# Performance work log

Measured on AMD Instinct MI355X. Metric: run time of the kernel, lower is better.

## Reference

```python
import jax, jax.numpy as jnp
import numpy as np

N, E, C, H, L, G, K, NC = 50000, 500000, 256, 128, 4, 64, 8, 2
EPS_MSG = 1e-7  # GENConv message eps
EPS_BN = 1e-5   # BatchNorm eps


def setup_inputs() -> dict:
    key = jax.random.key(0)
    ks = jax.random.split(key, 32)
    def nrm(k, shape, scale):
        return jax.random.normal(k, shape, dtype=jnp.float32) * scale
    sC = 1.0 / np.sqrt(C).astype(np.float32)
    sH = 1.0 / np.sqrt(H).astype(np.float32)
    s2H = 1.0 / np.sqrt(2 * H).astype(np.float32)
    return dict(
        x=nrm(ks[0], (N, C), 1.0),
        edge_index=jax.random.randint(ks[1], (2, E), 0, N, dtype=jnp.int32),
        edge_attr=jax.random.uniform(ks[2], (E, 1), dtype=jnp.float32),
        batch=jnp.sort(jax.random.randint(ks[3], (N,), 0, G, dtype=jnp.int32)),
        clinical=nrm(ks[4], (G, K), 1.0),
        lin_src_w=nrm(ks[5], (C, H), sC), lin_src_b=nrm(ks[6], (H,), 0.01),
        lin_dst_w=nrm(ks[7], (C, H), sC), lin_dst_b=nrm(ks[8], (H,), 0.01),
        edge_w=nrm(ks[9], (L, 1, H), 1.0), edge_b=nrm(ks[10], (L, H), 0.01),
        t=0.1 + 0.01 * jax.random.normal(ks[11], (L,), dtype=jnp.float32),
        mlp_w1=nrm(ks[12], (L, H, 2 * H), sH), mlp_b1=nrm(ks[13], (L, 2 * H), 0.01),
        mlp_bn_g=1.0 + nrm(ks[14], (L, 2 * H), 0.1), mlp_bn_b=nrm(ks[15], (L, 2 * H), 0.1),
        mlp_bn_m=nrm(ks[16], (L, 2 * H), 0.1),
        mlp_bn_v=1.0 + jax.random.uniform(ks[17], (L, 2 * H), dtype=jnp.float32),
        mlp_w2=nrm(ks[18], (L, 2 * H, H), s2H), mlp_b2=nrm(ks[19], (L, H), 0.01),
        norm_g=1.0 + nrm(ks[20], (L, H), 0.1), norm_b=nrm(ks[21], (L, H), 0.1),
        norm_m=nrm(ks[22], (L, H), 0.1),
        norm_v=1.0 + jax.random.uniform(ks[23], (L, H), dtype=jnp.float32),
        cls_w=nrm(ks[24], (H + K, NC), 1.0 / np.sqrt(H + K).astype(np.float32)),
        cls_b=nrm(ks[25], (NC,), 0.01),
    )


def _bn(h, g, b, m, v):
    # eval-mode BatchNorm with running stats
    return g * (h - m) * jax.lax.rsqrt(v + EPS_BN) + b


def reference(x, edge_index, edge_attr, batch, clinical,
              lin_src_w, lin_src_b, lin_dst_w, lin_dst_b,
              edge_w, edge_b, t,
              mlp_w1, mlp_b1, mlp_bn_g, mlp_bn_b, mlp_bn_m, mlp_bn_v,
              mlp_w2, mlp_b2, norm_g, norm_b, norm_m, norm_v,
              cls_w, cls_b):
    n = x.shape[0]
    g_count = clinical.shape[0]
    src, dst = edge_index[0], edge_index[1]
    n_layers = t.shape[0]

    def genconv(xs, xd, l):
        # xs: source features feeding messages [N,H]; xd: dst skip features [N,H]
        e = edge_attr @ edge_w[l] + edge_b[l]               # [E,H]
        msg = jax.nn.relu(xs[src] + e) + EPS_MSG            # [E,H]
        z = msg * t[l]
        zmax = jax.ops.segment_max(z, dst, num_segments=n)  # [N,H]
        zmax = jnp.where(jnp.isfinite(zmax), zmax, 0.0)
        ez = jnp.exp(z - zmax[dst])
        denom = jax.ops.segment_sum(ez, dst, num_segments=n)
        agg = jax.ops.segment_sum(msg * ez, dst, num_segments=n) / jnp.maximum(denom, 1e-16)
        out = agg + xd
        # internal MLP [H, 2H, H]: Linear -> BN -> ReLU -> Linear
        hmid = jax.nn.relu(_bn(out @ mlp_w1[l] + mlp_b1[l],
                               mlp_bn_g[l], mlp_bn_b[l], mlp_bn_m[l], mlp_bn_v[l]))
        return hmid @ mlp_w2[l] + mlp_b2[l]

    # layer 0: conv only (per DeepGCN.forward); lin_src / lin_dst project C -> H
    xs0 = x @ lin_src_w + lin_src_b
    xd0 = x @ lin_dst_w + lin_dst_b
    h = genconv(xs0, xd0, 0)

    # layers 1..L-1: res+ block (norm -> act -> conv, residual add); dropout = identity (eval)
    for l in range(1, n_layers):
        r = jax.nn.relu(_bn(h, norm_g[l], norm_b[l], norm_m[l], norm_v[l]))
        h = h + genconv(r, r, l)

    # final norm/act from layer 0
    h = jax.nn.relu(_bn(h, norm_g[0], norm_b[0], norm_m[0], norm_v[0]))

    # global mean pool over graphs
    cnt = jax.ops.segment_sum(jnp.ones((n,), h.dtype), batch, num_segments=g_count)
    pooled = jax.ops.segment_sum(h, batch, num_segments=g_count) / jnp.maximum(cnt, 1.0)[:, None]

    z = jnp.concatenate([pooled, clinical], axis=1)
    return z @ cls_w + cls_b  # [G, num_classes]; squeeze is a no-op for G>1, NC=2
```

## Files before the change

kernel.cpp:

```cpp
#include <hip/hip_runtime.h>
#include <math.h>

#define Nn 50000
#define MPAD 50048
#define Ee 500000
#define Cc 256
#define Hh 128
#define Ll 4
#define Gg 64
#define Kk 8
#define NCc 2

#define NB 196

typedef __attribute__((ext_vector_type(8))) short short8;
typedef __attribute__((ext_vector_type(4))) float f32x4;
typedef __attribute__((ext_vector_type(2))) float f32x2;

#define RFL __builtin_amdgcn_readfirstlane

__device__ __forceinline__ unsigned short f2bf(float f) {
    union { float f; unsigned int u; } v;
    v.f = f;
    unsigned int u = v.u;
    return (unsigned short)((u + 0x7FFFu + ((u >> 16) & 1u)) >> 16);
}
__device__ __forceinline__ float bf2f(unsigned short s) {
    union { float f; unsigned int u; } v;
    v.u = ((unsigned int)s) << 16;
    return v.f;
}
__device__ __forceinline__ float bf2f_lo(unsigned int u) {
    union { float f; unsigned int u; } v;
    v.u = u << 16;
    return v.f;
}
__device__ __forceinline__ float bf2f_hi(unsigned int u) {
    union { float f; unsigned int u; } v;
    v.u = u & 0xffff0000u;
    return v.f;
}


__global__ void hist_kernel(const int* __restrict__ dst, int* __restrict__ deg) {
    int e = blockIdx.x * 256 + threadIdx.x;
    if (e < Ee) atomicAdd(&deg[dst[e]], 1);
}

__global__ __launch_bounds__(256) void bsum_kernel(const int* __restrict__ deg,
                                                   int* __restrict__ bsum) {
    __shared__ int ws[4];
    int t = threadIdx.x;
    int i = blockIdx.x * 256 + t;
    int v = (i < Nn) ? deg[i] : 0;
#pragma unroll
    for (int o = 32; o; o >>= 1) v += __shfl_down(v, o, 64);
    if ((t & 63) == 0) ws[t >> 6] = v;
    __syncthreads();
    if (t == 0) bsum[blockIdx.x] = ws[0] + ws[1] + ws[2] + ws[3];
}

__global__ __launch_bounds__(256) void bscan_kernel(const int* __restrict__ bsum,
                                                    int* __restrict__ boff,
                                                    int* __restrict__ off) {
    __shared__ int sc[256];
    int t = threadIdx.x;
    int v = (t < NB) ? bsum[t] : 0;
    sc[t] = v;
    __syncthreads();
    for (int o = 1; o < 256; o <<= 1) {
        int u = (t >= o) ? sc[t - o] : 0;
        __syncthreads();
        sc[t] += u;
        __syncthreads();
    }
    if (t < NB) boff[t] = sc[t] - v;
    if (t == NB - 1) off[Nn] = sc[t];
}

__global__ __launch_bounds__(256) void offsets_kernel(const int* __restrict__ deg,
                                                      const int* __restrict__ boff,
                                                      int* __restrict__ off,
                                                      int* __restrict__ pos) {
    __shared__ int sc[256];
    int t = threadIdx.x;
    int i = blockIdx.x * 256 + t;
    int v = (i < Nn) ? deg[i] : 0;
    sc[t] = v;
    __syncthreads();
    for (int o = 1; o < 256; o <<= 1) {
        int u = (t >= o) ? sc[t - o] : 0;
        __syncthreads();
        sc[t] += u;
        __syncthreads();
    }
    int excl = sc[t] - v + boff[blockIdx.x];
    if (i < Nn) {
        off[i] = excl;
        pos[i] = excl;
    }
}

__global__ void scatter_kernel(const int* __restrict__ src, const int* __restrict__ dst,
                               const float* __restrict__ attr, int* __restrict__ pos,
                               int2* __restrict__ sedge) {
    int e = blockIdx.x * 256 + threadIdx.x;
    if (e < Ee) {
        int d = dst[e];
        int p = atomicAdd(&pos[d], 1);
        sedge[p] = make_int2(src[e], __float_as_int(attr[e]));
    }
}


__global__ void wconv_kernel(const float* __restrict__ lin_src_w,
                             const float* __restrict__ lin_dst_w,
                             const float* __restrict__ mlp_w1,
                             const float* __restrict__ mlp_w2,
                             unsigned short* __restrict__ wt) {
    int idx = blockIdx.x * 256 + threadIdx.x;
    if (idx >= 327680) return;
    float val;
    if (idx < 65536) {
        int n = idx >> 8, k = idx & 255;
        val = (n < 128) ? lin_src_w[k * 128 + n] : lin_dst_w[k * 128 + (n - 128)];
    } else if (idx < 196608) {
        int r = idx - 65536;
        int l = r >> 15, e = r & 32767;
        int n = e >> 7, k = e & 127;
        val = mlp_w1[(size_t)l * 32768 + k * 256 + n];
    } else {
        int r = idx - 196608;
        int l = r >> 15, e = r & 32767;
        int n = e >> 8, k = e & 255;
        val = mlp_w2[(size_t)l * 32768 + k * 128 + n];
    }
    wt[idx] = f2bf(val);
}


__global__ __launch_bounds__(256) void xconv_kernel(const float* __restrict__ x,
                                                    unsigned short* __restrict__ xbf) {
    int idx = blockIdx.x * 256 + threadIdx.x;
    if (idx >= (Nn * Cc) / 8) return;
    const float4* p = (const float4*)(x) + (size_t)idx * 2;
    float4 v0 = p[0], v1 = p[1];
    unsigned short t[8];
    t[0] = f2bf(v0.x); t[1] = f2bf(v0.y); t[2] = f2bf(v0.z); t[3] = f2bf(v0.w);
    t[4] = f2bf(v1.x); t[5] = f2bf(v1.y); t[6] = f2bf(v1.z); t[7] = f2bf(v1.w);
    *(short8*)(xbf + (size_t)idx * 8) = *(short8*)t;
}

#define GLOAD16(gp, lp)                                                                       \
    __builtin_amdgcn_global_load_lds(                                                         \
        (const __attribute__((address_space(1))) unsigned int*)(gp),                          \
        (__attribute__((address_space(3))) unsigned int*)(lp), 16, 0, 0)


__global__ __launch_bounds__(256) void proj_kernel(
    const unsigned short* __restrict__ A, const unsigned short* __restrict__ Bt,
    const float* __restrict__ bias, const float* __restrict__ bias2,
    unsigned short* __restrict__ Cout) {
    __shared__ __align__(16) unsigned short SH[24576];
    int tid = threadIdx.x;
    int wave = tid >> 6, lane = tid & 63;
    int wr = wave >> 1, wc = wave & 1;
    int lrow = lane & 15, quad = lane >> 4;
    int m0 = blockIdx.y * 128, n0 = blockIdx.x * 128;
    const int K = 256;

    const unsigned short* ag0 = A + (size_t)(m0 + (tid >> 2)) * K + (tid & 3) * 8;
    const unsigned short* ag1 = A + (size_t)(m0 + 64 + (tid >> 2)) * K + (tid & 3) * 8;
    const unsigned short* bg0 = Bt + (size_t)(n0 + (tid >> 2)) * K + (tid & 3) * 8;
    const unsigned short* bg1 = Bt + (size_t)(n0 + 64 + (tid >> 2)) * K + (tid & 3) * 8;

    f32x4 acc[4][4];
#pragma unroll
    for (int i = 0; i < 4; i++)
#pragma unroll
        for (int j = 0; j < 4; j++) acc[i][j] = (f32x4){0.f, 0.f, 0.f, 0.f};

    auto stage = [&](int buf, int koff) {
        GLOAD16(ag0 + koff, SH + buf * 4096 + wave * 512);
        GLOAD16(ag1 + koff, SH + buf * 4096 + 2048 + wave * 512);
        GLOAD16(bg0 + koff, SH + 12288 + buf * 4096 + wave * 512);
        GLOAD16(bg1 + koff, SH + 12288 + buf * 4096 + 2048 + wave * 512);
    };

    const int ntiles = 8;
    stage(0, 0);
    stage(1, 32);
    for (int t = 0; t < ntiles; ++t) {
        if (t + 1 < ntiles) {
            asm volatile("s_waitcnt vmcnt(4)\n\ts_barrier" ::: "memory");
        } else {
            asm volatile("s_waitcnt vmcnt(0)\n\ts_barrier" ::: "memory");
        }
        if (t + 2 < ntiles) stage((t + 2) % 3, (t + 2) * 32);
        int cur = t % 3;
        const unsigned short* As = SH + cur * 4096;
        const unsigned short* Bs = SH + 12288 + cur * 4096;
        short8 af[4], bfr[4];
#pragma unroll
        for (int mt = 0; mt < 4; mt++)
            af[mt] = *(const short8*)&As[(wr * 64 + mt * 16 + lrow) * 32 + quad * 8];
#pragma unroll
        for (int nf = 0; nf < 4; nf++)
            bfr[nf] = *(const short8*)&Bs[(wc * 64 + nf * 16 + lrow) * 32 + quad * 8];
#pragma unroll
        for (int mt = 0; mt < 4; mt++)
#pragma unroll
            for (int nf = 0; nf < 4; nf++)
                acc[mt][nf] = __builtin_amdgcn_mfma_f32_16x16x32_bf16(af[mt], bfr[nf],
                                                                     acc[mt][nf], 0, 0, 0);
    }

    __syncthreads();
    unsigned short* Cl = SH;
#pragma unroll
    for (int nf = 0; nf < 4; nf++) {
        int gc = n0 + wc * 64 + nf * 16 + lrow;
        float bs = (gc >= 128) ? bias2[gc - 128] : bias[gc];
        int col = wc * 64 + nf * 16 + lrow;
#pragma unroll
        for (int mt = 0; mt < 4; mt++)
#pragma unroll
            for (int r = 0; r < 4; r++)
                Cl[(wr * 64 + mt * 16 + quad * 4 + r) * 128 + col] = f2bf(acc[mt][nf][r] + bs);
    }
    __syncthreads();
#pragma unroll
    for (int p = 0; p < 8; p++) {
        int vid = p * 256 + tid;
        int row = vid >> 4, cg = (vid & 15) * 8;
        short8 v = *(const short8*)&Cl[row * 128 + cg];
        *(short8*)(Cout + (size_t)(m0 + row) * 256 + n0 + cg) = v;
    }
}


__global__ __launch_bounds__(256) void mlp_kernel(
    const unsigned short* __restrict__ A,
    const unsigned short* __restrict__ W1,
    const unsigned short* __restrict__ W2,
    const float* __restrict__ b1, const float* __restrict__ bn_g,
    const float* __restrict__ bn_b, const float* __restrict__ bn_m,
    const float* __restrict__ bn_v, const float* __restrict__ b2,
    const float* __restrict__ pn_g, const float* __restrict__ pn_b,
    const float* __restrict__ pn_m, const float* __restrict__ pn_v,
    float* __restrict__ hbuf, unsigned short* __restrict__ rbuf, int rmw) {
    __shared__ __align__(16) unsigned short Hm[64 * 264];

    int tid = threadIdx.x;
    int wave = tid >> 6, lane = tid & 63;
    int lrow = lane & 15, quad = lane >> 4;
    int m0 = blockIdx.x * 64;

    f32x4 acc1[4][4];
#pragma unroll
    for (int i = 0; i < 4; i++)
#pragma unroll
        for (int j = 0; j < 4; j++) acc1[i][j] = (f32x4){0.f, 0.f, 0.f, 0.f};
#pragma unroll
    for (int t = 0; t < 4; t++) {
        short8 af[4], bfr[4];
#pragma unroll
        for (int mt = 0; mt < 4; mt++)
            af[mt] = *(const short8*)(A + (size_t)(m0 + mt * 16 + lrow) * 128 +
                                      t * 32 + quad * 8);
#pragma unroll
        for (int nf = 0; nf < 4; nf++)
            bfr[nf] = *(const short8*)(W1 + (size_t)(wave * 64 + nf * 16 + lrow) * 128 +
                                       t * 32 + quad * 8);
#pragma unroll
        for (int mt = 0; mt < 4; mt++)
#pragma unroll
            for (int nf = 0; nf < 4; nf++)
                acc1[mt][nf] = __builtin_amdgcn_mfma_f32_16x16x32_bf16(af[mt], bfr[nf],
                                                                      acc1[mt][nf], 0, 0, 0);
    }
#pragma unroll
    for (int nf = 0; nf < 4; nf++) {
        int gc = wave * 64 + nf * 16 + lrow;
        float bs = b1[gc];
        float g = bn_g[gc], bb = bn_b[gc], mm = bn_m[gc];
        float inv = rsqrtf(bn_v[gc] + 1e-5f);
#pragma unroll
        for (int mt = 0; mt < 4; mt++)
#pragma unroll
            for (int r = 0; r < 4; r++) {
                float v = acc1[mt][nf][r] + bs;
                v = fmaxf(g * (v - mm) * inv + bb, 0.f);
                Hm[(mt * 16 + quad * 4 + r) * 264 + gc] = f2bf(v);
            }
    }
    __syncthreads();

    f32x4 acc2[4][2];
#pragma unroll
    for (int i = 0; i < 4; i++)
#pragma unroll
        for (int j = 0; j < 2; j++) acc2[i][j] = (f32x4){0.f, 0.f, 0.f, 0.f};
#pragma unroll
    for (int t = 0; t < 8; t++) {
        short8 af[4], bfr[2];
#pragma unroll
        for (int mt = 0; mt < 4; mt++)
            af[mt] = *(const short8*)&Hm[(mt * 16 + lrow) * 264 + t * 32 + quad * 8];
#pragma unroll
        for (int nf = 0; nf < 2; nf++)
            bfr[nf] = *(const short8*)(W2 + (size_t)(wave * 32 + nf * 16 + lrow) * 256 +
                                       t * 32 + quad * 8);
#pragma unroll
        for (int mt = 0; mt < 4; mt++)
#pragma unroll
            for (int nf = 0; nf < 2; nf++)
                acc2[mt][nf] = __builtin_amdgcn_mfma_f32_16x16x32_bf16(af[mt], bfr[nf],
                                                                      acc2[mt][nf], 0, 0, 0);
    }
    __syncthreads();

    float* C2 = (float*)Hm;
#pragma unroll
    for (int nf = 0; nf < 2; nf++) {
        int gc = wave * 32 + nf * 16 + lrow;
        float bs = b2[gc];
#pragma unroll
        for (int mt = 0; mt < 4; mt++)
#pragma unroll
            for (int r = 0; r < 4; r++)
                C2[(mt * 16 + quad * 4 + r) * 132 + gc] = acc2[mt][nf][r] + bs;
    }
    __syncthreads();
#pragma unroll
    for (int p = 0; p < 8; p++) {
        int vid = p * 256 + tid;
        int row = vid >> 5, c4 = (vid & 31) * 4;
        f32x4 v = *(const f32x4*)&C2[row * 132 + c4];
        float* hp = hbuf + (size_t)(m0 + row) * 128 + c4;
        if (rmw) v += *(const f32x4*)hp;
        *(f32x4*)hp = v;
        if (pn_g) {
            f32x4 pg = *(const f32x4*)&pn_g[c4];
            f32x4 pb = *(const f32x4*)&pn_b[c4];
            f32x4 pm = *(const f32x4*)&pn_m[c4];
            f32x4 pv = *(const f32x4*)&pn_v[c4];
            float r0 = fmaxf(pg[0] * (v[0] - pm[0]) * rsqrtf(pv[0] + 1e-5f) + pb[0], 0.f);
            float r1 = fmaxf(pg[1] * (v[1] - pm[1]) * rsqrtf(pv[1] + 1e-5f) + pb[1], 0.f);
            float r2 = fmaxf(pg[2] * (v[2] - pm[2]) * rsqrtf(pv[2] + 1e-5f) + pb[2], 0.f);
            float r3 = fmaxf(pg[3] * (v[3] - pm[3]) * rsqrtf(pv[3] + 1e-5f) + pb[3], 0.f);
            unsigned int w0 = (unsigned int)f2bf(r0) | ((unsigned int)f2bf(r1) << 16);
            unsigned int w1 = (unsigned int)f2bf(r2) | ((unsigned int)f2bf(r3) << 16);
            uint2 pk = make_uint2(w0, w1);
            *(uint2*)(rbuf + (size_t)(m0 + row) * 128 + c4) = pk;
        }
    }
}


template <int XSS>
__global__ __launch_bounds__(256) void agg_kernel(
    const unsigned short* __restrict__ xs,
    const unsigned short* __restrict__ xd, int xds,
    const int2* __restrict__ sedge, const int* __restrict__ off,
    const float* __restrict__ ew, const float* __restrict__ eb,
    const float* __restrict__ tptr, unsigned short* __restrict__ outb) {
    int wave = threadIdx.x >> 6;
    int lane = threadIdx.x & 63;
    int d0 = blockIdx.x * 8 + wave * 2;
    int d1 = d0 + 1;
    int f0 = lane * 2;
    unsigned int uda = *(const unsigned int*)(xd + (size_t)d0 * xds + f0);
    unsigned int udb = *(const unsigned int*)(xd + (size_t)d1 * xds + f0);
    f32x2 wv = *(const f32x2*)(ew + f0);
    f32x2 bv = *(const f32x2*)(eb + f0);
    float c = tptr[0] * 1.44269504088896f;
    const f32x2 zz = {0.f, 0.f};
    int s0a = RFL(off[d0]), s1a = RFL(off[d0 + 1]);
    int s0b = RFL(off[d1]), s1b = RFL(off[d1 + 1]);
    f32x2 dena = {0.f, 0.f}, numa = {0.f, 0.f};
    f32x2 denb = {0.f, 0.f}, numb = {0.f, 0.f};

#define EDGE2(u, av, den, num)                                      \
    {                                                               \
        f32x2 xv = {bf2f_lo(u), bf2f_hi(u)};                        \
        f32x2 m = __builtin_elementwise_max(xv + bv + (av)*wv, zz); \
        f32x2 e;                                                    \
        e.x = __builtin_amdgcn_exp2f(m.x * c);                      \
        e.y = __builtin_amdgcn_exp2f(m.y * c);                      \
        den += e;                                                   \
        num += m * e;                                               \
    }
#define EDGE2M(u, av, mk, den, num)                                 \
    {                                                               \
        f32x2 xv = {bf2f_lo(u), bf2f_hi(u)};                        \
        f32x2 m = __builtin_elementwise_max(xv + bv + (av)*wv, zz); \
        f32x2 e;                                                    \
        e.x = __builtin_amdgcn_exp2f(m.x * c) * (mk);               \
        e.y = __builtin_amdgcn_exp2f(m.y * c) * (mk);               \
        den += e;                                                   \
        num += m * e;                                               \
    }
#define LOADMETA(jv, ii, aa)                                   \
    {                                                          \
        int4 q0 = *(const int4*)(sedge + (jv));                \
        int4 q1 = *(const int4*)(sedge + (jv) + 2);            \
        int4 q2 = *(const int4*)(sedge + (jv) + 4);            \
        int4 q3 = *(const int4*)(sedge + (jv) + 6);            \
        ii[0] = RFL(q0.x); aa[0] = __int_as_float(RFL(q0.y));  \
        ii[1] = RFL(q0.z); aa[1] = __int_as_float(RFL(q0.w));  \
        ii[2] = RFL(q1.x); aa[2] = __int_as_float(RFL(q1.y));  \
        ii[3] = RFL(q1.z); aa[3] = __int_as_float(RFL(q1.w));  \
        ii[4] = RFL(q2.x); aa[4] = __int_as_float(RFL(q2.y));  \
        ii[5] = RFL(q2.z); aa[5] = __int_as_float(RFL(q2.w));  \
        ii[6] = RFL(q3.x); aa[6] = __int_as_float(RFL(q3.y));  \
        ii[7] = RFL(q3.z); aa[7] = __int_as_float(RFL(q3.w));  \
    }
#define GATHER8(ii, uu)                                                          \
    _Pragma("unroll") for (int k = 0; k < 8; k++) uu[k] =                        \
        *(const unsigned int*)(xs + (size_t)ii[k] * XSS + f0);

    int ja = s0a, jb = s0b;
    while (ja + 8 <= s1a && jb + 8 <= s1b) {
        int ia[8], ib[8];
        float aa[8], ab[8];
        LOADMETA(ja, ia, aa)
        LOADMETA(jb, ib, ab)
        unsigned int ua[8], ub[8];
        GATHER8(ia, ua)
        GATHER8(ib, ub)
#pragma unroll
        for (int k = 0; k < 8; k++) EDGE2(ua[k], aa[k], dena, numa)
#pragma unroll
        for (int k = 0; k < 8; k++) EDGE2(ub[k], ab[k], denb, numb)
        ja += 8;
        jb += 8;
    }
    while (ja + 8 <= s1a) {
        int ia[8];
        float aa[8];
        LOADMETA(ja, ia, aa)
        unsigned int ua[8];
        GATHER8(ia, ua)
#pragma unroll
        for (int k = 0; k < 8; k++) EDGE2(ua[k], aa[k], dena, numa)
        ja += 8;
    }
    while (jb + 8 <= s1b) {
        int ib[8];
        float ab[8];
        LOADMETA(jb, ib, ab)
        unsigned int ub[8];
        GATHER8(ib, ub)
#pragma unroll
        for (int k = 0; k < 8; k++) EDGE2(ub[k], ab[k], denb, numb)
        jb += 8;
    }
    if (ja < s1a || jb < s1b) {
        int lasta = (s1a > s0a) ? s1a - 1 : 0;
        int lastb = (s1b > s0b) ? s1b - 1 : 0;
        int ia[8], ib[8];
        float aa[8], ab[8], ma[8], mb[8];
#pragma unroll
        for (int k = 0; k < 8; k++) {
            int jj = ja + k;
            int cl = (jj < s1a) ? jj : lasta;
            int2 p = sedge[cl];
            ia[k] = RFL(p.x);
            aa[k] = __int_as_float(RFL(p.y));
            ma[k] = (jj < s1a) ? 1.f : 0.f;
            jj = jb + k;
            cl = (jj < s1b) ? jj : lastb;
            int2 q = sedge[cl];
            ib[k] = RFL(q.x);
            ab[k] = __int_as_float(RFL(q.y));
            mb[k] = (jj < s1b) ? 1.f : 0.f;
        }
        unsigned int ua[8], ub[8];
        GATHER8(ia, ua)
        GATHER8(ib, ub)
#pragma unroll
        for (int k = 0; k < 8; k++) EDGE2M(ua[k], aa[k], ma[k], dena, numa)
#pragma unroll
        for (int k = 0; k < 8; k++) EDGE2M(ub[k], ab[k], mb[k], denb, numb)
    }
#undef EDGE2
#undef EDGE2M
#undef LOADMETA
#undef GATHER8
    float a0 = (s1a > s0a) ? (numa.x / dena.x + 1e-7f) : 0.f;
    float a1 = (s1a > s0a) ? (numa.y / dena.y + 1e-7f) : 0.f;
    float b0 = (s1b > s0b) ? (numb.x / denb.x + 1e-7f) : 0.f;
    float b1 = (s1b > s0b) ? (numb.y / denb.y + 1e-7f) : 0.f;
    unsigned int lo = f2bf(a0 + bf2f_lo(uda));
    unsigned int hi = f2bf(a1 + bf2f_hi(uda));
    *(unsigned int*)(outb + (size_t)d0 * Hh + f0) = lo | (hi << 16);
    lo = f2bf(b0 + bf2f_lo(udb));
    hi = f2bf(b1 + bf2f_hi(udb));
    *(unsigned int*)(outb + (size_t)d1 * Hh + f0) = lo | (hi << 16);
}


#define PCHUNK 100

__global__ __launch_bounds__(128) void pool_kernel(
    const float* __restrict__ h, const int* __restrict__ batch,
    const float* __restrict__ g, const float* __restrict__ b,
    const float* __restrict__ m, const float* __restrict__ v,
    float* __restrict__ pooled, float* __restrict__ cnt) {
    int hh = threadIdx.x;
    int i0 = blockIdx.x * PCHUNK;
    int i1 = min(i0 + PCHUNK, Nn);
    if (i0 >= Nn) return;
    float gg = g[hh], bb = b[hh], mm = m[hh], inv = rsqrtf(v[hh] + 1e-5f);
    int cur = batch[i0];
    float sum = 0.f, c = 0.f;
    for (int i = i0; i < i1; i++) {
        int gid = batch[i];
        float val = fmaxf(gg * (h[(size_t)i * Hh + hh] - mm) * inv + bb, 0.f);
        if (gid != cur) {
            atomicAdd(&pooled[(size_t)cur * Hh + hh], sum);
            if (hh == 0) atomicAdd(&cnt[cur], c);
            cur = gid;
            sum = 0.f;
            c = 0.f;
        }
        sum += val;
        c += 1.f;
    }
    atomicAdd(&pooled[(size_t)cur * Hh + hh], sum);
    if (hh == 0) atomicAdd(&cnt[cur], c);
}


__global__ __launch_bounds__(128) void cls_kernel(const float* __restrict__ pooled,
                                                  const float* __restrict__ cnt,
                                                  const float* __restrict__ clinical,
                                                  const float* __restrict__ w,
                                                  const float* __restrict__ bias,
                                                  float* __restrict__ out) {
    int t = threadIdx.x;
    int g = t >> 1, c = t & 1;
    float inv = 1.f / fmaxf(cnt[g], 1.f);
    float s = bias[c];
    for (int j = 0; j < Hh; j++) s += pooled[g * Hh + j] * inv * w[j * NCc + c];
    for (int k = 0; k < Kk; k++) s += clinical[g * Kk + k] * w[(Hh + k) * NCc + c];
    out[g * NCc + c] = s;
}


extern "C" void kernel_launch(void* const* d_in, const int* in_sizes, int n_in,
                              void* d_out, int out_size, void* d_ws, size_t ws_size,
                              hipStream_t stream) {
    const float* x = (const float*)d_in[0];
    const int* eidx = (const int*)d_in[1];
    const float* eattr = (const float*)d_in[2];
    const int* batch = (const int*)d_in[3];
    const float* clinical = (const float*)d_in[4];
    const float* lin_src_w = (const float*)d_in[5];
    const float* lin_src_b = (const float*)d_in[6];
    const float* lin_dst_w = (const float*)d_in[7];
    const float* lin_dst_b = (const float*)d_in[8];
    const float* edge_w = (const float*)d_in[9];
    const float* edge_b = (const float*)d_in[10];
    const float* tt = (const float*)d_in[11];
    const float* mlp_w1 = (const float*)d_in[12];
    const float* mlp_b1 = (const float*)d_in[13];
    const float* bn_g = (const float*)d_in[14];
    const float* bn_b = (const float*)d_in[15];
    const float* bn_m = (const float*)d_in[16];
    const float* bn_v = (const float*)d_in[17];
    const float* mlp_w2 = (const float*)d_in[18];
    const float* mlp_b2 = (const float*)d_in[19];
    const float* norm_g = (const float*)d_in[20];
    const float* norm_b = (const float*)d_in[21];
    const float* norm_m = (const float*)d_in[22];
    const float* norm_v = (const float*)d_in[23];
    const float* cls_w = (const float*)d_in[24];
    const float* cls_b = (const float*)d_in[25];
    float* out = (float*)d_out;

    const int* src = eidx;
    const int* dst = eidx + Ee;

    char* ws = (char*)d_ws;
    size_t off_b = 0;
    auto alloc = [&](size_t bytes) -> void* {
        void* p = ws + off_b;
        off_b += (bytes + 255) & ~(size_t)255;
        return p;
    };
    unsigned short* xsd = (unsigned short*)alloc((size_t)MPAD * 256 * 2);
    unsigned short* rbuf = (unsigned short*)alloc((size_t)MPAD * Hh * 2);
    unsigned short* aggout = (unsigned short*)alloc((size_t)MPAD * Hh * 2);
    unsigned short* xbf = (unsigned short*)alloc((size_t)MPAD * 256 * 2);
    float* hbuf = (float*)alloc((size_t)MPAD * Hh * 4);
    int* deg = (int*)alloc((Nn + 1) * 4);
    int* offp = (int*)alloc((Nn + 1) * 4);
    int* pos = (int*)alloc((size_t)Nn * 4);
    int* bsum = (int*)alloc(NB * 4);
    int* boff = (int*)alloc(NB * 4);
    int2* sedge = (int2*)alloc((size_t)Ee * 8);
    float* pooled = (float*)alloc((size_t)Gg * Hh * 4);
    float* cntb = (float*)alloc(Gg * 4);
    unsigned short* wt = (unsigned short*)alloc((size_t)327680 * 2);

    hipMemsetAsync(deg, 0, (Nn + 1) * 4, stream);
    hipMemsetAsync(pooled, 0, (size_t)Gg * Hh * 4, stream);
    hipMemsetAsync(cntb, 0, Gg * 4, stream);

    hist_kernel<<<(Ee + 255) / 256, 256, 0, stream>>>(dst, deg);
    bsum_kernel<<<NB, 256, 0, stream>>>(deg, bsum);
    bscan_kernel<<<1, 256, 0, stream>>>(bsum, boff, offp);
    offsets_kernel<<<NB, 256, 0, stream>>>(deg, boff, offp, pos);
    scatter_kernel<<<(Ee + 255) / 256, 256, 0, stream>>>(src, dst, eattr, pos, sedge);
    wconv_kernel<<<1280, 256, 0, stream>>>(lin_src_w, lin_dst_w, mlp_w1, mlp_w2, wt);
    xconv_kernel<<<(Nn * Cc / 8 + 255) / 256, 256, 0, stream>>>(x, xbf);

    const unsigned short* wt_proj = wt;
    const unsigned short* wt_w1 = wt + 65536;
    const unsigned short* wt_w2 = wt + 196608;

    dim3 gproj(2, MPAD / 128);
    proj_kernel<<<gproj, 256, 0, stream>>>(xbf, wt_proj, lin_src_b, lin_dst_b, xsd);

    for (int l = 0; l < Ll; l++) {
        if (l == 0) {
            agg_kernel<256><<<Nn / 8, 256, 0, stream>>>(xsd, xsd + 128, 256, sedge, offp,
                                                        edge_w + l * Hh, edge_b + l * Hh,
                                                        tt + l, aggout);
        } else {
            agg_kernel<128><<<Nn / 8, 256, 0, stream>>>(rbuf, rbuf, Hh, sedge, offp,
                                                        edge_w + l * Hh, edge_b + l * Hh,
                                                        tt + l, aggout);
        }
        const float* png = (l < Ll - 1) ? (norm_g + (l + 1) * Hh) : nullptr;
        const float* pnb = (l < Ll - 1) ? (norm_b + (l + 1) * Hh) : nullptr;
        const float* pnm = (l < Ll - 1) ? (norm_m + (l + 1) * Hh) : nullptr;
        const float* pnv = (l < Ll - 1) ? (norm_v + (l + 1) * Hh) : nullptr;
        mlp_kernel<<<MPAD / 64, 256, 0, stream>>>(
            aggout, wt_w1 + (size_t)l * 32768, wt_w2 + (size_t)l * 32768,
            mlp_b1 + l * 2 * Hh, bn_g + l * 2 * Hh, bn_b + l * 2 * Hh,
            bn_m + l * 2 * Hh, bn_v + l * 2 * Hh, mlp_b2 + l * Hh,
            png, pnb, pnm, pnv, hbuf, rbuf, (l == 0) ? 0 : 1);
    }

    pool_kernel<<<(Nn + PCHUNK - 1) / PCHUNK, 128, 0, stream>>>(hbuf, batch, norm_g, norm_b,
                                                                norm_m, norm_v, pooled, cntb);
    cls_kernel<<<1, 128, 0, stream>>>(pooled, cntb, clinical, cls_w, cls_b, out);
}
```

Measured before the change: 528.1 us.

## Stage MLP GEMM operands through double-buffered LDS with async global loads

The fused MLP kernel no longer loads A, W1 and W2 fragments straight from global memory into registers. It copies each 32-wide K slice into a double-buffered shared-memory area with GLOAD16 and prefetches the next slice while MFMAs run on the current one. This is meant to hide global load latency and read uncoalesced fragments from LDS instead of global memory. The cost is an extra 40 KB of LDS, which may lower occupancy, plus a __syncthreads per K step. The output staging also moves to the new buffer with an unpadded stride of 128, which may add bank conflicts.

```diff
diff --git a/kernel.cpp b/kernel.cpp
--- a/kernel.cpp
+++ b/kernel.cpp
@@ -249,6 +249,7 @@
     const float* __restrict__ pn_g, const float* __restrict__ pn_b,
     const float* __restrict__ pn_m, const float* __restrict__ pn_v,
     float* __restrict__ hbuf, unsigned short* __restrict__ rbuf, int rmw) {
+    __shared__ __align__(16) unsigned short S[20480];
     __shared__ __align__(16) unsigned short Hm[64 * 264];
 
     int tid = threadIdx.x;
@@ -256,29 +257,46 @@
     int lrow = lane & 15, quad = lane >> 4;
     int m0 = blockIdx.x * 64;
 
+    const unsigned short* ag = A + (size_t)(m0 + (tid >> 2)) * 128 + (tid & 3) * 8;
+    const unsigned short* bg = W1 + (size_t)(tid >> 2) * 128 + (tid & 3) * 8;
+
     f32x4 acc1[4][4];
 #pragma unroll
     for (int i = 0; i < 4; i++)
 #pragma unroll
         for (int j = 0; j < 4; j++) acc1[i][j] = (f32x4){0.f, 0.f, 0.f, 0.f};
-#pragma unroll
-    for (int t = 0; t < 4; t++) {
+
+    auto stage1 = [&](int buf, int k0) {
+        GLOAD16(ag + k0, S + buf * 2048 + wave * 512);
+#pragma unroll
+        for (int c = 0; c < 4; c++)
+            GLOAD16(bg + (size_t)c * 64 * 128 + k0,
+                    S + 4096 + buf * 8192 + c * 2048 + wave * 512);
+    };
+
+    stage1(0, 0);
+    __syncthreads();
+    for (int t = 0; t < 4; ++t) {
+        if (t + 1 < 4) stage1((t + 1) & 1, (t + 1) * 32);
+        int cur = t & 1;
+        const unsigned short* A1s = S + cur * 2048;
+        const unsigned short* B1s = S + 4096 + cur * 8192;
         short8 af[4], bfr[4];
 #pragma unroll
         for (int mt = 0; mt < 4; mt++)
-            af[mt] = *(const short8*)(A + (size_t)(m0 + mt * 16 + lrow) * 128 +
-                                      t * 32 + quad * 8);
+            af[mt] = *(const short8*)&A1s[(mt * 16 + lrow) * 32 + quad * 8];
 #pragma unroll
         for (int nf = 0; nf < 4; nf++)
-            bfr[nf] = *(const short8*)(W1 + (size_t)(wave * 64 + nf * 16 + lrow) * 128 +
-                                       t * 32 + quad * 8);
+            bfr[nf] = *(const short8*)&B1s[(wave * 64 + nf * 16 + lrow) * 32 + quad * 8];
 #pragma unroll
         for (int mt = 0; mt < 4; mt++)
 #pragma unroll
             for (int nf = 0; nf < 4; nf++)
                 acc1[mt][nf] = __builtin_amdgcn_mfma_f32_16x16x32_bf16(af[mt], bfr[nf],
                                                                       acc1[mt][nf], 0, 0, 0);
-    }
+        __syncthreads();
+    }
+
 #pragma unroll
     for (int nf = 0; nf < 4; nf++) {
         int gc = wave * 64 + nf * 16 + lrow;
@@ -296,31 +314,43 @@
     }
     __syncthreads();
 
+    const unsigned short* b2g0 = W2 + (size_t)(tid >> 2) * 256 + (tid & 3) * 8;
+    const unsigned short* b2g1 = W2 + (size_t)(64 + (tid >> 2)) * 256 + (tid & 3) * 8;
+
     f32x4 acc2[4][2];
 #pragma unroll
     for (int i = 0; i < 4; i++)
 #pragma unroll
         for (int j = 0; j < 2; j++) acc2[i][j] = (f32x4){0.f, 0.f, 0.f, 0.f};
-#pragma unroll
-    for (int t = 0; t < 8; t++) {
+
+    auto stage2 = [&](int buf, int k0) {
+        GLOAD16(b2g0 + k0, S + buf * 4096 + wave * 512);
+        GLOAD16(b2g1 + k0, S + buf * 4096 + 2048 + wave * 512);
+    };
+
+    stage2(0, 0);
+    __syncthreads();
+    for (int t = 0; t < 8; ++t) {
+        if (t + 1 < 8) stage2((t + 1) & 1, (t + 1) * 32);
+        int cur = t & 1;
+        const unsigned short* B2s = S + cur * 4096;
         short8 af[4], bfr[2];
 #pragma unroll
         for (int mt = 0; mt < 4; mt++)
             af[mt] = *(const short8*)&Hm[(mt * 16 + lrow) * 264 + t * 32 + quad * 8];
 #pragma unroll
         for (int nf = 0; nf < 2; nf++)
-            bfr[nf] = *(const short8*)(W2 + (size_t)(wave * 32 + nf * 16 + lrow) * 256 +
-                                       t * 32 + quad * 8);
+            bfr[nf] = *(const short8*)&B2s[(wave * 32 + nf * 16 + lrow) * 32 + quad * 8];
 #pragma unroll
         for (int mt = 0; mt < 4; mt++)
 #pragma unroll
             for (int nf = 0; nf < 2; nf++)
                 acc2[mt][nf] = __builtin_amdgcn_mfma_f32_16x16x32_bf16(af[mt], bfr[nf],
                                                                       acc2[mt][nf], 0, 0, 0);
-    }
-    __syncthreads();
-
-    float* C2 = (float*)Hm;
+        __syncthreads();
+    }
+
+    float* C2 = (float*)S;
 #pragma unroll
     for (int nf = 0; nf < 2; nf++) {
         int gc = wave * 32 + nf * 16 + lrow;
@@ -329,14 +359,14 @@
         for (int mt = 0; mt < 4; mt++)
 #pragma unroll
             for (int r = 0; r < 4; r++)
-                C2[(mt * 16 + quad * 4 + r) * 132 + gc] = acc2[mt][nf][r] + bs;
+                C2[(mt * 16 + quad * 4 + r) * 128 + gc] = acc2[mt][nf][r] + bs;
     }
     __syncthreads();
 #pragma unroll
     for (int p = 0; p < 8; p++) {
         int vid = p * 256 + tid;
         int row = vid >> 5, c4 = (vid & 31) * 4;
-        f32x4 v = *(const f32x4*)&C2[row * 132 + c4];
+        f32x4 v = *(const f32x4*)&C2[row * 128 + c4];
         float* hp = hbuf + (size_t)(m0 + row) * 128 + c4;
         if (rmw) v += *(const f32x4*)hp;
         *(f32x4*)hp = v;
```

Result: faster. 495.5 us (-6.2%).

## Stage MLP weight panels through LDS with triple-buffered async loads

Applied to the files above, without the earlier changes.

Rewrites the fused MLP kernel so the A tile and the W1/W2 panels are prefetched into shared memory with async global-to-LDS loads (GLOAD16), using a three-slot ring buffer and vmcnt waits plus barriers. Previously each wave read its weight fragments straight from global memory inside the MFMA loop. Each GEMM is now split into two output halves, which lowers live accumulator registers per wave. Separately, the workspace allocations are reordered so that deg, pooled and cntb sit next to each other and can be cleared with a single memset instead of three. The cost is more barriers and hand-counted waitcnt logic that must match the number of loads issued.

```diff
diff --git a/kernel.cpp b/kernel.cpp
--- a/kernel.cpp
+++ b/kernel.cpp
@@ -249,39 +249,98 @@
     const float* __restrict__ pn_g, const float* __restrict__ pn_b,
     const float* __restrict__ pn_m, const float* __restrict__ pn_v,
     float* __restrict__ hbuf, unsigned short* __restrict__ rbuf, int rmw) {
-    __shared__ __align__(16) unsigned short Hm[64 * 264];
+    __shared__ __align__(16) unsigned short LDS_[23040];
+    unsigned short* Ap = LDS_;
+    unsigned short* B1 = LDS_ + 8192;
+    unsigned short* Hm = LDS_;
+    unsigned short* B2 = LDS_ + 16896;
 
     int tid = threadIdx.x;
     int wave = tid >> 6, lane = tid & 63;
     int lrow = lane & 15, quad = lane >> 4;
     int m0 = blockIdx.x * 64;
 
-    f32x4 acc1[4][4];
+    {
+        const unsigned short* as = A + (size_t)(m0 + (tid >> 2)) * 128 + (tid & 3) * 8;
+#pragma unroll
+        for (int t = 0; t < 4; t++) GLOAD16(as + t * 32, Ap + t * 2048 + wave * 512);
+    }
+    const unsigned short* w1base = W1 + (size_t)(tid >> 2) * 128 + (tid & 3) * 8;
+    auto stageB1 = [&](int s, int b) {
+        int h = s >> 2, t = s & 3;
+        const unsigned short* p = w1base + (size_t)h * 128 * 128 + t * 32;
+        GLOAD16(p, B1 + b * 4096 + wave * 512);
+        GLOAD16(p + (size_t)64 * 128, B1 + b * 4096 + 2048 + wave * 512);
+    };
+    stageB1(0, 0);
+    stageB1(1, 1);
+
+    f32x4 acc1a[4][2], acc1b[4][2];
 #pragma unroll
     for (int i = 0; i < 4; i++)
 #pragma unroll
-        for (int j = 0; j < 4; j++) acc1[i][j] = (f32x4){0.f, 0.f, 0.f, 0.f};
+        for (int j = 0; j < 2; j++) {
+            acc1a[i][j] = (f32x4){0.f, 0.f, 0.f, 0.f};
+            acc1b[i][j] = (f32x4){0.f, 0.f, 0.f, 0.f};
+        }
+
 #pragma unroll
     for (int t = 0; t < 4; t++) {
-        short8 af[4], bfr[4];
-#pragma unroll
-        for (int mt = 0; mt < 4; mt++)
-            af[mt] = *(const short8*)(A + (size_t)(m0 + mt * 16 + lrow) * 128 +
-                                      t * 32 + quad * 8);
-#pragma unroll
-        for (int nf = 0; nf < 4; nf++)
-            bfr[nf] = *(const short8*)(W1 + (size_t)(wave * 64 + nf * 16 + lrow) * 128 +
-                                       t * 32 + quad * 8);
-#pragma unroll
-        for (int mt = 0; mt < 4; mt++)
-#pragma unroll
-            for (int nf = 0; nf < 4; nf++)
-                acc1[mt][nf] = __builtin_amdgcn_mfma_f32_16x16x32_bf16(af[mt], bfr[nf],
-                                                                      acc1[mt][nf], 0, 0, 0);
-    }
-#pragma unroll
-    for (int nf = 0; nf < 4; nf++) {
-        int gc = wave * 64 + nf * 16 + lrow;
+        asm volatile("s_waitcnt vmcnt(2)\n\ts_barrier" ::: "memory");
+        stageB1(t + 2, (t + 2) % 3);
+        const unsigned short* Apan = Ap + t * 2048;
+        const unsigned short* Bs = B1 + (t % 3) * 4096;
+        short8 af[4], bfr[2];
+#pragma unroll
+        for (int mt = 0; mt < 4; mt++)
+            af[mt] = *(const short8*)&Apan[(mt * 16 + lrow) * 32 + quad * 8];
+#pragma unroll
+        for (int nf = 0; nf < 2; nf++)
+            bfr[nf] = *(const short8*)&Bs[(wave * 32 + nf * 16 + lrow) * 32 + quad * 8];
+#pragma unroll
+        for (int mt = 0; mt < 4; mt++)
+#pragma unroll
+            for (int nf = 0; nf < 2; nf++)
+                acc1a[mt][nf] = __builtin_amdgcn_mfma_f32_16x16x32_bf16(af[mt], bfr[nf],
+                                                                       acc1a[mt][nf], 0, 0, 0);
+    }
+#pragma unroll
+    for (int t = 0; t < 4; t++) {
+        if (t < 3) {
+            asm volatile("s_waitcnt vmcnt(2)\n\ts_barrier" ::: "memory");
+        } else {
+            asm volatile("s_waitcnt vmcnt(0)\n\ts_barrier" ::: "memory");
+        }
+        if (t < 2) stageB1(6 + t, (6 + t) % 3);
+        const unsigned short* Apan = Ap + t * 2048;
+        const unsigned short* Bs = B1 + ((4 + t) % 3) * 4096;
+        short8 af[4], bfr[2];
+#pragma unroll
+        for (int mt = 0; mt < 4; mt++)
+            af[mt] = *(const short8*)&Apan[(mt * 16 + lrow) * 32 + quad * 8];
+#pragma unroll
+        for (int nf = 0; nf < 2; nf++)
+            bfr[nf] = *(const short8*)&Bs[(wave * 32 + nf * 16 + lrow) * 32 + quad * 8];
+#pragma unroll
+        for (int mt = 0; mt < 4; mt++)
+#pragma unroll
+            for (int nf = 0; nf < 2; nf++)
+                acc1b[mt][nf] = __builtin_amdgcn_mfma_f32_16x16x32_bf16(af[mt], bfr[nf],
+                                                                       acc1b[mt][nf], 0, 0, 0);
+    }
+    __syncthreads();
+
+    const unsigned short* w2base = W2 + (size_t)(tid >> 2) * 256 + (tid & 3) * 8;
+    auto stageB2 = [&](int s, int b) {
+        int h = s >> 3, t = s & 7;
+        GLOAD16(w2base + (size_t)h * 64 * 256 + t * 32, B2 + b * 2048 + wave * 512);
+    };
+    stageB2(0, 0);
+    stageB2(1, 1);
+
+#pragma unroll
+    for (int nf = 0; nf < 2; nf++) {
+        int gc = wave * 32 + nf * 16 + lrow;
         float bs = b1[gc];
         float g = bn_g[gc], bb = bn_b[gc], mm = bn_m[gc];
         float inv = rsqrtf(bn_v[gc] + 1e-5f);
@@ -289,47 +348,79 @@
         for (int mt = 0; mt < 4; mt++)
 #pragma unroll
             for (int r = 0; r < 4; r++) {
-                float v = acc1[mt][nf][r] + bs;
+                float v = acc1a[mt][nf][r] + bs;
                 v = fmaxf(g * (v - mm) * inv + bb, 0.f);
                 Hm[(mt * 16 + quad * 4 + r) * 264 + gc] = f2bf(v);
             }
     }
-    __syncthreads();
-
-    f32x4 acc2[4][2];
-#pragma unroll
-    for (int i = 0; i < 4; i++)
-#pragma unroll
-        for (int j = 0; j < 2; j++) acc2[i][j] = (f32x4){0.f, 0.f, 0.f, 0.f};
+#pragma unroll
+    for (int nf = 0; nf < 2; nf++) {
+        int gc = 128 + wave * 32 + nf * 16 + lrow;
+        float bs = b1[gc];
+        float g = bn_g[gc], bb = bn_b[gc], mm = bn_m[gc];
+        float inv = rsqrtf(bn_v[gc] + 1e-5f);
+#pragma unroll
+        for (int mt = 0; mt < 4; mt++)
+#pragma unroll
+            for (int r = 0; r < 4; r++) {
+                float v = acc1b[mt][nf][r] + bs;
+                v = fmaxf(g * (v - mm) * inv + bb, 0.f);
+                Hm[(mt * 16 + quad * 4 + r) * 264 + gc] = f2bf(v);
+            }
+    }
+    __syncthreads();
+
+    f32x4 acc2a[4], acc2b[4];
+#pragma unroll
+    for (int i = 0; i < 4; i++) {
+        acc2a[i] = (f32x4){0.f, 0.f, 0.f, 0.f};
+        acc2b[i] = (f32x4){0.f, 0.f, 0.f, 0.f};
+    }
 #pragma unroll
     for (int t = 0; t < 8; t++) {
-        short8 af[4], bfr[2];
+        asm volatile("s_waitcnt vmcnt(1)\n\ts_barrier" ::: "memory");
+        stageB2(t + 2, (t + 2) % 3);
+        const unsigned short* Bs = B2 + (t % 3) * 2048;
+        short8 af[4];
 #pragma unroll
         for (int mt = 0; mt < 4; mt++)
             af[mt] = *(const short8*)&Hm[(mt * 16 + lrow) * 264 + t * 32 + quad * 8];
-#pragma unroll
-        for (int nf = 0; nf < 2; nf++)
-            bfr[nf] = *(const short8*)(W2 + (size_t)(wave * 32 + nf * 16 + lrow) * 256 +
-                                       t * 32 + quad * 8);
-#pragma unroll
-        for (int mt = 0; mt < 4; mt++)
-#pragma unroll
-            for (int nf = 0; nf < 2; nf++)
-                acc2[mt][nf] = __builtin_amdgcn_mfma_f32_16x16x32_bf16(af[mt], bfr[nf],
-                                                                      acc2[mt][nf], 0, 0, 0);
-    }
-    __syncthreads();
-
-    float* C2 = (float*)Hm;
-#pragma unroll
-    for (int nf = 0; nf < 2; nf++) {
-        int gc = wave * 32 + nf * 16 + lrow;
-        float bs = b2[gc];
-#pragma unroll
-        for (int mt = 0; mt < 4; mt++)
-#pragma unroll
-            for (int r = 0; r < 4; r++)
-                C2[(mt * 16 + quad * 4 + r) * 132 + gc] = acc2[mt][nf][r] + bs;
+        short8 bf = *(const short8*)&Bs[(wave * 16 + lrow) * 32 + quad * 8];
+#pragma unroll
+        for (int mt = 0; mt < 4; mt++)
+            acc2a[mt] = __builtin_amdgcn_mfma_f32_16x16x32_bf16(af[mt], bf, acc2a[mt], 0, 0, 0);
+    }
+#pragma unroll
+    for (int t = 0; t < 8; t++) {
+        if (t < 7) {
+            asm volatile("s_waitcnt vmcnt(1)\n\ts_barrier" ::: "memory");
+        } else {
+            asm volatile("s_waitcnt vmcnt(0)\n\ts_barrier" ::: "memory");
+        }
+        if (t < 6) stageB2(10 + t, (10 + t) % 3);
+        const unsigned short* Bs = B2 + ((8 + t) % 3) * 2048;
+        short8 af[4];
+#pragma unroll
+        for (int mt = 0; mt < 4; mt++)
+            af[mt] = *(const short8*)&Hm[(mt * 16 + lrow) * 264 + t * 32 + quad * 8];
+        short8 bf = *(const short8*)&Bs[(wave * 16 + lrow) * 32 + quad * 8];
+#pragma unroll
+        for (int mt = 0; mt < 4; mt++)
+            acc2b[mt] = __builtin_amdgcn_mfma_f32_16x16x32_bf16(af[mt], bf, acc2b[mt], 0, 0, 0);
+    }
+    __syncthreads();
+
+    float* C2 = (float*)LDS_;
+    {
+        int gc0 = wave * 16 + lrow, gc1 = 64 + wave * 16 + lrow;
+        float bs0 = b2[gc0], bs1 = b2[gc1];
+#pragma unroll
+        for (int mt = 0; mt < 4; mt++)
+#pragma unroll
+            for (int r = 0; r < 4; r++) {
+                C2[(mt * 16 + quad * 4 + r) * 132 + gc0] = acc2a[mt][r] + bs0;
+                C2[(mt * 16 + quad * 4 + r) * 132 + gc1] = acc2b[mt][r] + bs1;
+            }
     }
     __syncthreads();
 #pragma unroll
@@ -590,24 +681,22 @@
         off_b += (bytes + 255) & ~(size_t)255;
         return p;
     };
+    int* deg = (int*)alloc((Nn + 1) * 4);
+    float* pooled = (float*)alloc((size_t)Gg * Hh * 4);
+    float* cntb = (float*)alloc(Gg * 4);
     unsigned short* xsd = (unsigned short*)alloc((size_t)MPAD * 256 * 2);
     unsigned short* rbuf = (unsigned short*)alloc((size_t)MPAD * Hh * 2);
     unsigned short* aggout = (unsigned short*)alloc((size_t)MPAD * Hh * 2);
     unsigned short* xbf = (unsigned short*)alloc((size_t)MPAD * 256 * 2);
     float* hbuf = (float*)alloc((size_t)MPAD * Hh * 4);
-    int* deg = (int*)alloc((Nn + 1) * 4);
     int* offp = (int*)alloc((Nn + 1) * 4);
     int* pos = (int*)alloc((size_t)Nn * 4);
     int* bsum = (int*)alloc(NB * 4);
     int* boff = (int*)alloc(NB * 4);
     int2* sedge = (int2*)alloc((size_t)Ee * 8);
-    float* pooled = (float*)alloc((size_t)Gg * Hh * 4);
-    float* cntb = (float*)alloc(Gg * 4);
     unsigned short* wt = (unsigned short*)alloc((size_t)327680 * 2);
 
-    hipMemsetAsync(deg, 0, (Nn + 1) * 4, stream);
-    hipMemsetAsync(pooled, 0, (size_t)Gg * Hh * 4, stream);
-    hipMemsetAsync(cntb, 0, Gg * 4, stream);
+    hipMemsetAsync(deg, 0, 200192 + 32768 + 256, stream);
 
     hist_kernel<<<(Ee + 255) / 256, 256, 0, stream>>>(dst, deg);
     bsum_kernel<<<NB, 256, 0, stream>>>(deg, bsum);
```

Measured after the change: 492.3 us, median of 2. 1.07x faster.
